# Optimization experiments

Measured on AMD Instinct MI355X. Metric: run time of the kernel, lower is better.

The kernel has to match this reference:

```python
import jax, jax.numpy as jnp
import numpy as np

WH, WW = 7, 7
SH, SW = 3, 3
NUM_HEADS = 8


def _rel_pos_index(wh, ww):
    coords = np.stack(np.meshgrid(np.arange(wh), np.arange(ww), indexing='ij')).reshape(2, -1)
    rel = (coords[:, :, None] - coords[:, None, :]).transpose(1, 2, 0)  # [N,N,2]
    rel[..., 0] += wh - 1
    rel[..., 1] += ww - 1
    rel[..., 0] *= 2 * ww - 1
    return rel.sum(-1)  # [N,N] int


def _attn_mask(Hp, Wp, wh, ww, sh, sw):
    img = np.zeros((Hp, Wp), dtype=np.float32)
    cnt = 0
    for hs in (slice(0, -wh), slice(-wh, -sh), slice(-sh, None)):
        for ws in (slice(0, -ww), slice(-ww, -sw), slice(-sw, None)):
            img[hs, ws] = cnt
            cnt += 1
    win = img.reshape(Hp // wh, wh, Wp // ww, ww).transpose(0, 2, 1, 3).reshape(-1, wh * ww)  # [nW,N]
    diff = win[:, None, :] - win[:, :, None]  # [nW,N,N]
    return np.where(diff != 0, -100.0, 0.0).astype(np.float32)


def _layernorm(x, g, b, eps=1e-5):
    mu = jnp.mean(x, -1, keepdims=True)
    var = jnp.mean(jnp.square(x - mu), -1, keepdims=True)
    return (x - mu) * jax.lax.rsqrt(var + eps) * g + b


def setup_inputs() -> dict:
    key = jax.random.key(0)
    ks = jax.random.split(key, 12)
    B, H, W, C = 32, 56, 56, 256
    hid = 4 * C
    s = lambda k, *shape: jax.random.normal(k, shape, jnp.float32) * 0.02
    return {
        'x': jax.random.normal(ks[0], (B, H * W, C), jnp.float32),
        'g1': jnp.ones((C,), jnp.float32), 'b1': jnp.zeros((C,), jnp.float32),
        'qkv_w': s(ks[1], 3 * C, C), 'qkv_b': jnp.zeros((3 * C,), jnp.float32),
        'bias_table': s(ks[2], (2 * WH - 1) * (2 * WW - 1), NUM_HEADS),
        'proj_w': s(ks[3], C, C), 'proj_b': jnp.zeros((C,), jnp.float32),
        'g2': jnp.ones((C,), jnp.float32), 'b2': jnp.zeros((C,), jnp.float32),
        'w1': s(ks[4], hid, C), 'bm1': jnp.zeros((hid,), jnp.float32),
        'w2': s(ks[5], C, hid), 'bm2': jnp.zeros((C,), jnp.float32),
        'H': H, 'W': W,
    }


def reference(x, g1, b1, qkv_w, qkv_b, bias_table, proj_w, proj_b, g2, b2, w1, bm1, w2, bm2, H, W):
    B, L, C = x.shape
    wh, ww = WH, WW
    nH = NUM_HEADS
    hd = C // nH
    scale = hd ** -0.5
    N = wh * ww

    shortcut = x
    h = _layernorm(x, g1, b1).reshape(B, H, W, C)
    pad_b = (wh - H % wh) % wh
    pad_r = (ww - W % ww) % ww
    if pad_b or pad_r:
        h = jnp.pad(h, ((0, 0), (0, pad_b), (0, pad_r), (0, 0)))
    Hp, Wp = h.shape[1], h.shape[2]

    h = jnp.roll(h, (-SH, -SW), axis=(1, 2))
    # window partition -> [B*nW, N, C]
    nWh, nWw = Hp // wh, Wp // ww
    xw = h.reshape(B, nWh, wh, nWw, ww, C).transpose(0, 1, 3, 2, 4, 5).reshape(-1, N, C)

    qkv = jnp.einsum('bnc,oc->bno', xw, qkv_w) + qkv_b  # [B*nW, N, 3C]
    qkv = qkv.reshape(-1, N, 3, nH, hd).transpose(2, 0, 3, 1, 4)
    q, k, v = qkv[0] * scale, qkv[1], qkv[2]  # [B*nW, nH, N, hd]
    attn = jnp.einsum('whnd,whmd->whnm', q, k)  # [B*nW, nH, N, N]

    rpi = jnp.asarray(_rel_pos_index(wh, ww))
    bias = bias_table[rpi.reshape(-1)].reshape(N, N, nH).transpose(2, 0, 1)  # [nH,N,N]
    attn = attn + bias[None]

    mask = jnp.asarray(_attn_mask(Hp, Wp, wh, ww, SH, SW))  # [nW,N,N]
    nW = mask.shape[0]
    attn = attn.reshape(B, nW, nH, N, N) + mask[None, :, None]
    attn = jax.nn.softmax(attn.reshape(-1, nH, N, N), axis=-1)

    out = jnp.einsum('whnm,whmd->whnd', attn, v).transpose(0, 2, 1, 3).reshape(-1, N, C)
    out = jnp.einsum('bnc,oc->bno', out, proj_w) + proj_b

    # window reverse
    out = out.reshape(B, nWh, nWw, wh, ww, C).transpose(0, 1, 3, 2, 4, 5).reshape(B, Hp, Wp, C)
    out = jnp.roll(out, (SH, SW), axis=(1, 2))
    if pad_b or pad_r:
        out = out[:, :H, :W, :]
    out = out.reshape(B, H * W, C)

    x = shortcut + out
    m = _layernorm(x, g2, b2)
    m = jax.nn.gelu(jnp.einsum('blc,oc->blo', m, w1) + bm1, approximate=False)
    m = jnp.einsum('blh,oh->blo', m, w2) + bm2
    return x + m
```

## Files before the change

kernel.cpp:

```cpp
#include <hip/hip_runtime.h>
#include <hip/hip_bf16.h>

#define DEVI __device__ __forceinline__
#define AS1 __attribute__((address_space(1)))
#define AS3 __attribute__((address_space(3)))

typedef short bf16x8 __attribute__((ext_vector_type(8)));
typedef float f32x4  __attribute__((ext_vector_type(4)));

constexpr int MROWS = 100352;

DEVI int win_row_to_token(int r) {
  int b   = r / 3136;
  int rem = r - b * 3136;
  int wi  = rem / 49;
  int t   = rem - wi * 49;
  int nwh = wi >> 3, nww = wi & 7;
  int th = t / 7, tw = t - th * 7;
  int h = nwh * 7 + th + 3; if (h >= 56) h -= 56;
  int w = nww * 7 + tw + 3; if (w >= 56) w -= 56;
  return b * 3136 + h * 56 + w;
}

DEVI unsigned short f2bf(float f) {
  __hip_bfloat16 h = __float2bfloat16(f);
  return __builtin_bit_cast(unsigned short, h);
}

__global__ void cvt_kernel(const float* __restrict__ in, __hip_bfloat16* __restrict__ out, int n) {
  int i = blockIdx.x * 256 + threadIdx.x;
  if (i < n) out[i] = __float2bfloat16(in[i]);
}

template<bool WIN>
__global__ __launch_bounds__(256) void ln_kernel(
    const float* __restrict__ xin, const float* __restrict__ g,
    const float* __restrict__ b, __hip_bfloat16* __restrict__ outb)
{
  int r = blockIdx.x * 4 + (threadIdx.x >> 6);
  int l = threadIdx.x & 63;
  int tok = WIN ? win_row_to_token(r) : r;
  float4 xv = *(const float4*)&xin[(size_t)tok * 256 + l * 4];
  float s = xv.x + xv.y + xv.z + xv.w;
  float q = xv.x * xv.x + xv.y * xv.y + xv.z * xv.z + xv.w * xv.w;
  #pragma unroll
  for (int off = 32; off; off >>= 1) { s += __shfl_xor(s, off); q += __shfl_xor(q, off); }
  float mu = s * (1.0f / 256.0f);
  float var = q * (1.0f / 256.0f) - mu * mu;
  float rs = rsqrtf(var + 1e-5f);
  float4 gv = *(const float4*)&g[l * 4];
  float4 bv = *(const float4*)&b[l * 4];
  ushort4 st;
  st.x = f2bf((xv.x - mu) * rs * gv.x + bv.x);
  st.y = f2bf((xv.y - mu) * rs * gv.y + bv.y);
  st.z = f2bf((xv.z - mu) * rs * gv.z + bv.z);
  st.w = f2bf((xv.w - mu) * rs * gv.w + bv.w);
  *(ushort4*)&outb[(size_t)r * 256 + l * 4] = st;
}

enum { EPI_QKV = 0, EPI_PROJ = 1, EPI_MLP1 = 2, EPI_MLP2 = 3 };

template<int EPI, int KTOT>
__global__ __launch_bounds__(512, 1) void strip3(
    const __hip_bfloat16* __restrict__ A,
    const __hip_bfloat16* __restrict__ Bw,
    int ntiles,
    const float* __restrict__ bias,
    const float* __restrict__ xres,
    float* __restrict__ outf,
    __hip_bfloat16* __restrict__ outb)
{
  constexpr int NKB = KTOT / 256;
  constexpr int NCH = NKB * 4;
  constexpr long TSTRIDE = 256L * KTOT * 2;
  __shared__ __align__(16) __hip_bfloat16 Bl[128 * 256];
  __shared__ __align__(16) __hip_bfloat16 Al[2][256 * 64];

  const int tid = threadIdx.x;
  const int w = tid >> 6, l = tid & 63;
  const int wr = w >> 1, wc = w & 1;
  const int g = l >> 4, lm = l & 15;

  const int xcd = blockIdx.x & 7;
  const int cu  = blockIdx.x >> 3;
  const int T   = 49 * ntiles;
  const int t0  = (cu * T) >> 5;
  const int t1  = ((cu + 1) * T) >> 5;

  char* AlB = (char*)&Al[0][0];
  char* BlB = (char*)&Bl[0];

  const int  dstW = w * 1024;
  const long aoff = (long)(w * 8 + (l >> 3)) * (KTOT * 2) + (((l & 7) ^ (l >> 3)) << 4);
  const int  bA   = wr * 8192  + lm * 128 + ((g ^ (lm & 7)) << 4);
  const int  bB   = wc * 32768 + lm * 512 + ((g ^ (lm & 7)) << 4);

  int nt = t0 / 49;
  int mtoff = t0 - nt * 49;
  const char* Ab = (const char*)A;
  const char* At = Ab + (long)(xcd * 49 + mtoff) * TSTRIDE;

  auto issueA = [&](const char* Atile, int coff, int buf) {
    #pragma unroll
    for (int j = 0; j < 4; ++j)
      __builtin_amdgcn_global_load_lds(
          (const AS1 void*)(Atile + aoff + j * (64L * KTOT * 2) + coff),
          (AS3 void*)(AlB + buf * 32768 + j * 8192 + dstW), 16, 0, 0);
  };
  auto stageB = [&](int nt_, int kb_) {
    const char* Bb = (const char*)(Bw + (size_t)nt_ * 128 * KTOT + kb_ * 256);
    #pragma unroll
    for (int j = 0; j < 8; ++j) {
      int U = j * 512 + w * 64 + l;
      int row = U >> 5;
      int su = (U & 31) ^ (row & 7);
      __builtin_amdgcn_global_load_lds(
          (const AS1 void*)(Bb + (long)row * (KTOT * 2) + su * 16),
          (AS3 void*)(BlB + j * 8192 + dstW), 16, 0, 0);
    }
  };

  stageB(nt, 0);
  int sBnt = nt, sBkb = 0;
  issueA(At, 0, 0);

  f32x4 acc[4][4];
  for (int t = t0; t < t1; ++t) {
    const bool wrap = (mtoff == 48);
    const char* Atn = wrap ? (Ab + (long)(xcd * 49) * TSTRIDE) : (At + TSTRIDE);
    #pragma unroll
    for (int mi = 0; mi < 4; ++mi)
      #pragma unroll
      for (int ni = 0; ni < 4; ++ni)
        acc[mi][ni] = f32x4{0.f, 0.f, 0.f, 0.f};

    #pragma unroll
    for (int kb = 0; kb < NKB; ++kb) {
      if (sBnt != nt || sBkb != kb) { stageB(nt, kb); sBnt = nt; sBkb = kb; }
      #pragma unroll
      for (int c = 0; c < 4; ++c) {
        const int chunk = kb * 4 + c;
        if (chunk == NCH - 1) {
          if (t == t1 - 1) {
            asm volatile("s_waitcnt vmcnt(0)" ::: "memory");
          } else {
            issueA(Atn, 0, 0);
            asm volatile("s_waitcnt vmcnt(4)" ::: "memory");
          }
        } else {
          issueA(At, (chunk + 1) * 128, (chunk + 1) & 1);
          asm volatile("s_waitcnt vmcnt(4)" ::: "memory");
        }
        __builtin_amdgcn_s_barrier();
        asm volatile("" ::: "memory");

        #pragma unroll
        for (int kk = 0; kk < 2; ++kk) {
          bf16x8 af[4], bf[4];
          const int ax = bA ^ (kk * 64);
          const int bx = bB ^ (kk * 64);
          #pragma unroll
          for (int mi = 0; mi < 4; ++mi)
            af[mi] = *(const bf16x8*)(AlB + (chunk & 1) * 32768 + ax + mi * 2048);
          #pragma unroll
          for (int ni = 0; ni < 4; ++ni)
            bf[ni] = *(const bf16x8*)(BlB + bx + c * 128 + ni * 8192);
          #pragma unroll
          for (int mi = 0; mi < 4; ++mi)
            #pragma unroll
            for (int ni = 0; ni < 4; ++ni)
              acc[mi][ni] = __builtin_amdgcn_mfma_f32_16x16x32_bf16(
                  af[mi], bf[ni], acc[mi][ni], 0, 0, 0);
        }
        asm volatile("" ::: "memory");
        __builtin_amdgcn_s_barrier();
      }
    }

    {
      const int mt = xcd * 49 + mtoff;
      #pragma unroll
      for (int mi = 0; mi < 4; ++mi)
        #pragma unroll
        for (int j = 0; j < 4; ++j) {
          int grow = mt * 256 + wr * 64 + mi * 16 + g * 4 + j;
          int orow = grow;
          if (EPI == EPI_PROJ) orow = win_row_to_token(grow);
          #pragma unroll
          for (int ni = 0; ni < 4; ++ni) {
            int gcol = nt * 128 + wc * 64 + ni * 16 + lm;
            float v = acc[mi][ni][j] + bias[gcol];
            if (EPI == EPI_QKV) {
              outb[(size_t)grow * 768 + gcol] = __float2bfloat16(v);
            } else if (EPI == EPI_PROJ) {
              size_t o = (size_t)orow * 256 + gcol;
              outf[o] = xres[o] + v;
            } else if (EPI == EPI_MLP1) {
              float u2 = v * (1.5957691216f + 0.1426930877f * v * v);
              float e  = __expf(u2);
              float ge = v * e / (e + 1.0f);
              outb[(size_t)grow * 1024 + gcol] = __float2bfloat16(ge);
            } else {
              size_t o = (size_t)grow * 256 + gcol;
              outf[o] += v;
            }
          }
        }
    }

    At = Atn;
    if (wrap) { mtoff = 0; ++nt; } else { ++mtoff; }
  }
}

__global__ __launch_bounds__(256) void bias_prep_kernel(
    const float* __restrict__ bt, float* __restrict__ Sadd)
{
  int blk = blockIdx.x;
  int cls = blk >> 3, h = blk & 7;
  int re = cls >> 1, ce = cls & 1;
  int lane = threadIdx.x & 63, fs = threadIdx.x >> 6;
  int g = lane >> 4, lm = lane & 15;
  #pragma unroll
  for (int i = 0; i < 4; ++i) {
    int f = fs * 4 + i;
    int mi = f >> 2, ni = f & 3;
    int key = ni * 16 + lm;
    f32x4 v;
    #pragma unroll
    for (int j = 0; j < 4; ++j) {
      int q = mi * 16 + g * 4 + j;
      float val;
      if (key >= 49) {
        val = -1e30f;
      } else {
        int qq = q > 48 ? 48 : q;
        int qh = qq / 7, qw = qq - qh * 7;
        int kh = key / 7, kw = key - kh * 7;
        int rpi = (qh - kh + 6) * 13 + (qw - kw + 6);
        val = bt[rpi * 8 + h];
        int rq = (re ? (qh < 4 ? 1 : 2) : 0) * 3 + (ce ? (qw < 4 ? 1 : 2) : 0);
        int rk = (re ? (kh < 4 ? 1 : 2) : 0) * 3 + (ce ? (kw < 4 ? 1 : 2) : 0);
        if (rq != rk) val -= 100.0f;
      }
      v[j] = val;
    }
    ((f32x4*)Sadd)[(blk * 16 + f) * 64 + lane] = v;
  }
}

__global__ __launch_bounds__(256) void attn_mfma_kernel(
    const __hip_bfloat16* __restrict__ qkv,
    const float* __restrict__ Sadd,
    __hip_bfloat16* __restrict__ attn_out)
{
  __shared__ __align__(16) __hip_bfloat16 Pl[4][64 * 72];
  int blk = blockIdx.x;
  int win = blk >> 1, half = blk & 1;
  int w = threadIdx.x >> 6, l = threadIdx.x & 63;
  int head = half * 4 + w;
  int g = l >> 4, lm = l & 15;
  int wi = win & 63;
  int cls = (((wi >> 3) == 7) ? 2 : 0) | (((wi & 7) == 7) ? 1 : 0);
  const __hip_bfloat16* base = qkv + (size_t)win * 49 * 768 + head * 32;

  bf16x8 aQ[4], bK[4];
  #pragma unroll
  for (int mi = 0; mi < 4; ++mi) {
    int q = mi * 16 + lm; if (q > 48) q = 48;
    aQ[mi] = *(const bf16x8*)(base + q * 768 + g * 8);
  }
  #pragma unroll
  for (int ni = 0; ni < 4; ++ni) {
    int k = ni * 16 + lm; if (k > 48) k = 48;
    bK[ni] = *(const bf16x8*)(base + 256 + k * 768 + g * 8);
  }
  f32x4 acc[4][4] = {};
  #pragma unroll
  for (int mi = 0; mi < 4; ++mi)
    #pragma unroll
    for (int ni = 0; ni < 4; ++ni)
      acc[mi][ni] = __builtin_amdgcn_mfma_f32_16x16x32_bf16(aQ[mi], bK[ni], acc[mi][ni], 0, 0, 0);

  const float scale = 0.17677669529663687f;
  const f32x4* Sb = (const f32x4*)Sadd + (size_t)(cls * 8 + head) * 16 * 64 + l;

  f32x4 rsum[4];
  __hip_bfloat16* P = Pl[w];
  #pragma unroll
  for (int mi = 0; mi < 4; ++mi) {
    #pragma unroll
    for (int ni = 0; ni < 4; ++ni) {
      f32x4 sv = Sb[(mi * 4 + ni) * 64];
      #pragma unroll
      for (int j = 0; j < 4; ++j) acc[mi][ni][j] = acc[mi][ni][j] * scale + sv[j];
    }
    f32x4 mx = acc[mi][0];
    #pragma unroll
    for (int ni = 1; ni < 4; ++ni)
      #pragma unroll
      for (int j = 0; j < 4; ++j) mx[j] = fmaxf(mx[j], acc[mi][ni][j]);
    #pragma unroll
    for (int msk = 1; msk < 16; msk <<= 1)
      #pragma unroll
      for (int j = 0; j < 4; ++j) mx[j] = fmaxf(mx[j], __shfl_xor(mx[j], msk));
    f32x4 sm = {};
    #pragma unroll
    for (int ni = 0; ni < 4; ++ni)
      #pragma unroll
      for (int j = 0; j < 4; ++j) {
        float e = __expf(acc[mi][ni][j] - mx[j]);
        acc[mi][ni][j] = e;
        sm[j] += e;
      }
    #pragma unroll
    for (int msk = 1; msk < 16; msk <<= 1)
      #pragma unroll
      for (int j = 0; j < 4; ++j) sm[j] += __shfl_xor(sm[j], msk);
    rsum[mi] = sm;
    #pragma unroll
    for (int ni = 0; ni < 4; ++ni)
      #pragma unroll
      for (int j = 0; j < 4; ++j) {
        int q = mi * 16 + g * 4 + j;
        int key = ni * 16 + lm;
        P[q * 72 + key] = __float2bfloat16(acc[mi][ni][j]);
      }
  }

  bf16x8 bV[2][2];
  #pragma unroll
  for (int s = 0; s < 2; ++s)
    #pragma unroll
    for (int n2 = 0; n2 < 2; ++n2) {
      bf16x8 vv;
      #pragma unroll
      for (int e = 0; e < 8; ++e) {
        int key = s * 32 + g * 8 + e; if (key > 48) key = 48;
        vv[e] = __builtin_bit_cast(short, base[512 + key * 768 + n2 * 16 + lm]);
      }
      bV[s][n2] = vv;
    }

  f32x4 o[4][2] = {};
  #pragma unroll
  for (int s = 0; s < 2; ++s)
    #pragma unroll
    for (int mi2 = 0; mi2 < 4; ++mi2) {
      bf16x8 aP = *(const bf16x8*)&P[(mi2 * 16 + lm) * 72 + s * 32 + g * 8];
      #pragma unroll
      for (int n2 = 0; n2 < 2; ++n2)
        o[mi2][n2] = __builtin_amdgcn_mfma_f32_16x16x32_bf16(aP, bV[s][n2], o[mi2][n2], 0, 0, 0);
    }

  #pragma unroll
  for (int mi2 = 0; mi2 < 4; ++mi2) {
    f32x4 li;
    #pragma unroll
    for (int j = 0; j < 4; ++j) li[j] = 1.0f / rsum[mi2][j];
    #pragma unroll
    for (int n2 = 0; n2 < 2; ++n2)
      #pragma unroll
      for (int j = 0; j < 4; ++j) {
        int q = mi2 * 16 + g * 4 + j;
        if (q < 49)
          attn_out[((size_t)win * 49 + q) * 256 + head * 32 + n2 * 16 + lm] =
              __float2bfloat16(o[mi2][n2][j] * li[j]);
      }
  }
}

extern "C" void kernel_launch(void* const* d_in, const int* in_sizes, int n_in,
                              void* d_out, int out_size, void* d_ws, size_t ws_size,
                              hipStream_t stream) {
  const float* x          = (const float*)d_in[0];
  const float* g1         = (const float*)d_in[1];
  const float* b1         = (const float*)d_in[2];
  const float* qkv_w      = (const float*)d_in[3];
  const float* qkv_b      = (const float*)d_in[4];
  const float* bias_table = (const float*)d_in[5];
  const float* proj_w     = (const float*)d_in[6];
  const float* proj_b     = (const float*)d_in[7];
  const float* g2         = (const float*)d_in[8];
  const float* b2         = (const float*)d_in[9];
  const float* w1         = (const float*)d_in[10];
  const float* bm1        = (const float*)d_in[11];
  const float* w2         = (const float*)d_in[12];
  const float* bm2        = (const float*)d_in[13];
  float* out = (float*)d_out;

  char* ws = (char*)d_ws;
  __hip_bfloat16* A_ln   = (__hip_bfloat16*)(ws);
  __hip_bfloat16* qkvb   = (__hip_bfloat16*)(ws + 51380224);
  __hip_bfloat16* attn_o = (__hip_bfloat16*)(ws + 205520896);
  __hip_bfloat16* hidden = qkvb;
  __hip_bfloat16* qkv_wb  = (__hip_bfloat16*)(ws + 256901120);
  __hip_bfloat16* proj_wb = qkv_wb + 196608;
  __hip_bfloat16* w1b     = proj_wb + 65536;
  __hip_bfloat16* w2b     = w1b + 262144;
  float* Sadd = (float*)(ws + 258473984);

  cvt_kernel<<<(196608 + 255) / 256, 256, 0, stream>>>(qkv_w, qkv_wb, 196608);
  cvt_kernel<<<(65536  + 255) / 256, 256, 0, stream>>>(proj_w, proj_wb, 65536);
  cvt_kernel<<<(262144 + 255) / 256, 256, 0, stream>>>(w1, w1b, 262144);
  cvt_kernel<<<(262144 + 255) / 256, 256, 0, stream>>>(w2, w2b, 262144);
  bias_prep_kernel<<<32, 256, 0, stream>>>(bias_table, Sadd);

  ln_kernel<true><<<MROWS / 4, 256, 0, stream>>>(x, g1, b1, A_ln);

  strip3<EPI_QKV, 256><<<256, 512, 0, stream>>>(
      A_ln, qkv_wb, 6, qkv_b, nullptr, nullptr, qkvb);

  attn_mfma_kernel<<<4096, 256, 0, stream>>>(qkvb, Sadd, attn_o);

  strip3<EPI_PROJ, 256><<<256, 512, 0, stream>>>(
      attn_o, proj_wb, 2, proj_b, x, out, nullptr);

  ln_kernel<false><<<MROWS / 4, 256, 0, stream>>>(out, g2, b2, A_ln);

  strip3<EPI_MLP1, 256><<<256, 512, 0, stream>>>(
      A_ln, w1b, 8, bm1, nullptr, nullptr, hidden);

  strip3<EPI_MLP2, 1024><<<256, 512, 0, stream>>>(
      hidden, w2b, 2, bm2, nullptr, out, nullptr);
}
```

Measured before the change: 498.7 us.

## Shrink GEMM strip tiles to 128 rows with 256-thread blocks, single-buffered A

The persistent strip GEMM goes from 512-thread blocks with 256-row M tiles to 256-thread blocks with 128-row tiles, launched as 512 blocks so two can share a CU. The A tile is now single-buffered. The wait is a full vmcnt(0) plus barrier before each chunk, and the next chunk's loads (and the next B strip) are issued only after compute finishes. The aim is overlap across co-resident blocks rather than within one block, with smaller LDS per block. The cost is that latency is no longer hidden inside a block, and B is re-staged more often relative to the work done.

```diff
diff --git a/kernel.cpp b/kernel.cpp
--- a/kernel.cpp
+++ b/kernel.cpp
@@ -61,7 +61,7 @@
 enum { EPI_QKV = 0, EPI_PROJ = 1, EPI_MLP1 = 2, EPI_MLP2 = 3 };
 
 template<int EPI, int KTOT>
-__global__ __launch_bounds__(512, 1) void strip3(
+__global__ __launch_bounds__(256) void strip4(
     const __hip_bfloat16* __restrict__ A,
     const __hip_bfloat16* __restrict__ Bw,
     int ntiles,
@@ -72,9 +72,10 @@
 {
   constexpr int NKB = KTOT / 256;
   constexpr int NCH = NKB * 4;
-  constexpr long TSTRIDE = 256L * KTOT * 2;
+  constexpr int K2  = KTOT * 2;
+  constexpr long TSTRIDE = 128L * K2;
   __shared__ __align__(16) __hip_bfloat16 Bl[128 * 256];
-  __shared__ __align__(16) __hip_bfloat16 Al[2][256 * 64];
+  __shared__ __align__(16) __hip_bfloat16 Al[128 * 64];
 
   const int tid = threadIdx.x;
   const int w = tid >> 6, l = tid & 63;
@@ -82,52 +83,49 @@
   const int g = l >> 4, lm = l & 15;
 
   const int xcd = blockIdx.x & 7;
-  const int cu  = blockIdx.x >> 3;
-  const int T   = 49 * ntiles;
-  const int t0  = (cu * T) >> 5;
-  const int t1  = ((cu + 1) * T) >> 5;
-
-  char* AlB = (char*)&Al[0][0];
-  char* BlB = (char*)&Bl[0];
+  const int cu2 = blockIdx.x >> 3;
+  const int T   = 98 * ntiles;
+  const int t0  = (cu2 * T) >> 6;
+  const int t1  = ((cu2 + 1) * T) >> 6;
+
+  char* AlB = (char*)Al;
+  char* BlB = (char*)Bl;
 
   const int  dstW = w * 1024;
-  const long aoff = (long)(w * 8 + (l >> 3)) * (KTOT * 2) + (((l & 7) ^ (l >> 3)) << 4);
-  const int  bA   = wr * 8192  + lm * 128 + ((g ^ (lm & 7)) << 4);
-  const int  bB   = wc * 32768 + lm * 512 + ((g ^ (lm & 7)) << 4);
-
-  int nt = t0 / 49;
-  int mtoff = t0 - nt * 49;
-  const char* Ab = (const char*)A;
-  const char* At = Ab + (long)(xcd * 49 + mtoff) * TSTRIDE;
-
-  auto issueA = [&](const char* Atile, int coff, int buf) {
+  const long aoff = (long)(tid >> 3) * K2 + (((tid & 7) ^ ((tid >> 3) & 7)) << 4);
+  const long boff = (long)(tid >> 5) * K2 + (((tid & 31) ^ ((tid >> 5) & 7)) << 4);
+  const int  bA = (wr * 64 + lm) * 128 + ((g ^ (lm & 7)) << 4);
+  const int  bB = (wc * 64 + lm) * 512 + ((g ^ (lm & 7)) << 4);
+
+  int nt = t0 / 98;
+  int mtoff = t0 - nt * 98;
+  const char* Ab = (const char*)A + (long)xcd * 98 * TSTRIDE;
+  const char* At = Ab + (long)mtoff * TSTRIDE;
+
+  auto issueA = [&](const char* Atile, int ch) {
     #pragma unroll
     for (int j = 0; j < 4; ++j)
       __builtin_amdgcn_global_load_lds(
-          (const AS1 void*)(Atile + aoff + j * (64L * KTOT * 2) + coff),
-          (AS3 void*)(AlB + buf * 32768 + j * 8192 + dstW), 16, 0, 0);
+          (const AS1 void*)(Atile + aoff + j * (32L * K2) + ch * 128),
+          (AS3 void*)(AlB + j * 4096 + dstW), 16, 0, 0);
   };
   auto stageB = [&](int nt_, int kb_) {
-    const char* Bb = (const char*)(Bw + (size_t)nt_ * 128 * KTOT + kb_ * 256);
-    #pragma unroll
-    for (int j = 0; j < 8; ++j) {
-      int U = j * 512 + w * 64 + l;
-      int row = U >> 5;
-      int su = (U & 31) ^ (row & 7);
+    const char* Bb = (const char*)Bw + (long)nt_ * 128 * K2 + kb_ * 512;
+    #pragma unroll
+    for (int j = 0; j < 16; ++j)
       __builtin_amdgcn_global_load_lds(
-          (const AS1 void*)(Bb + (long)row * (KTOT * 2) + su * 16),
-          (AS3 void*)(BlB + j * 8192 + dstW), 16, 0, 0);
-    }
+          (const AS1 void*)(Bb + boff + j * (8L * K2)),
+          (AS3 void*)(BlB + j * 4096 + dstW), 16, 0, 0);
   };
 
   stageB(nt, 0);
-  int sBnt = nt, sBkb = 0;
-  issueA(At, 0, 0);
+  issueA(At, 0);
 
   f32x4 acc[4][4];
   for (int t = t0; t < t1; ++t) {
-    const bool wrap = (mtoff == 48);
-    const char* Atn = wrap ? (Ab + (long)(xcd * 49) * TSTRIDE) : (At + TSTRIDE);
+    const bool wrap = (mtoff == 97);
+    const char* Atn = wrap ? Ab : (At + TSTRIDE);
+    const int ntn = wrap ? nt + 1 : nt;
     #pragma unroll
     for (int mi = 0; mi < 4; ++mi)
       #pragma unroll
@@ -136,35 +134,24 @@
 
     #pragma unroll
     for (int kb = 0; kb < NKB; ++kb) {
-      if (sBnt != nt || sBkb != kb) { stageB(nt, kb); sBnt = nt; sBkb = kb; }
-      #pragma unroll
-      for (int c = 0; c < 4; ++c) {
-        const int chunk = kb * 4 + c;
-        if (chunk == NCH - 1) {
-          if (t == t1 - 1) {
-            asm volatile("s_waitcnt vmcnt(0)" ::: "memory");
-          } else {
-            issueA(Atn, 0, 0);
-            asm volatile("s_waitcnt vmcnt(4)" ::: "memory");
-          }
-        } else {
-          issueA(At, (chunk + 1) * 128, (chunk + 1) & 1);
-          asm volatile("s_waitcnt vmcnt(4)" ::: "memory");
-        }
+      #pragma unroll
+      for (int c4 = 0; c4 < 4; ++c4) {
+        const int ch = kb * 4 + c4;
+        asm volatile("s_waitcnt vmcnt(0)" ::: "memory");
         __builtin_amdgcn_s_barrier();
         asm volatile("" ::: "memory");
 
         #pragma unroll
         for (int kk = 0; kk < 2; ++kk) {
           bf16x8 af[4], bf[4];
-          const int ax = bA ^ (kk * 64);
-          const int bx = bB ^ (kk * 64);
+          const int ax = bA ^ (kk << 6);
+          const int bx = bB ^ (kk << 6);
           #pragma unroll
           for (int mi = 0; mi < 4; ++mi)
-            af[mi] = *(const bf16x8*)(AlB + (chunk & 1) * 32768 + ax + mi * 2048);
+            af[mi] = *(const bf16x8*)(AlB + ax + mi * 2048);
           #pragma unroll
           for (int ni = 0; ni < 4; ++ni)
-            bf[ni] = *(const bf16x8*)(BlB + bx + c * 128 + ni * 8192);
+            bf[ni] = *(const bf16x8*)(BlB + bx + c4 * 128 + ni * 8192);
           #pragma unroll
           for (int mi = 0; mi < 4; ++mi)
             #pragma unroll
@@ -172,18 +159,27 @@
               acc[mi][ni] = __builtin_amdgcn_mfma_f32_16x16x32_bf16(
                   af[mi], bf[ni], acc[mi][ni], 0, 0, 0);
         }
+
         asm volatile("" ::: "memory");
         __builtin_amdgcn_s_barrier();
+        if (ch < NCH - 1) {
+          if (NKB > 1 && c4 == 3) stageB(nt, kb + 1);
+          issueA(At, ch + 1);
+        } else if (t < t1 - 1) {
+          if (NKB > 1) stageB(ntn, 0);
+          else if (ntn != nt) stageB(ntn, 0);
+          issueA(Atn, 0);
+        }
       }
     }
 
     {
-      const int mt = xcd * 49 + mtoff;
+      const int mt = xcd * 98 + mtoff;
       #pragma unroll
       for (int mi = 0; mi < 4; ++mi)
         #pragma unroll
         for (int j = 0; j < 4; ++j) {
-          int grow = mt * 256 + wr * 64 + mi * 16 + g * 4 + j;
+          int grow = mt * 128 + wr * 64 + mi * 16 + g * 4 + j;
           int orow = grow;
           if (EPI == EPI_PROJ) orow = win_row_to_token(grow);
           #pragma unroll
@@ -209,7 +205,7 @@
     }
 
     At = Atn;
-    if (wrap) { mtoff = 0; ++nt; } else { ++mtoff; }
+    if (wrap) { mtoff = 0; nt = ntn; } else { ++mtoff; }
   }
 }
 
@@ -408,19 +404,19 @@
 
   ln_kernel<true><<<MROWS / 4, 256, 0, stream>>>(x, g1, b1, A_ln);
 
-  strip3<EPI_QKV, 256><<<256, 512, 0, stream>>>(
+  strip4<EPI_QKV, 256><<<512, 256, 0, stream>>>(
       A_ln, qkv_wb, 6, qkv_b, nullptr, nullptr, qkvb);
 
   attn_mfma_kernel<<<4096, 256, 0, stream>>>(qkvb, Sadd, attn_o);
 
-  strip3<EPI_PROJ, 256><<<256, 512, 0, stream>>>(
+  strip4<EPI_PROJ, 256><<<512, 256, 0, stream>>>(
       attn_o, proj_wb, 2, proj_b, x, out, nullptr);
 
   ln_kernel<false><<<MROWS / 4, 256, 0, stream>>>(out, g2, b2, A_ln);
 
-  strip3<EPI_MLP1, 256><<<256, 512, 0, stream>>>(
+  strip4<EPI_MLP1, 256><<<512, 256, 0, stream>>>(
       A_ln, w1b, 8, bm1, nullptr, nullptr, hidden);
 
-  strip3<EPI_MLP2, 1024><<<256, 512, 0, stream>>>(
+  strip4<EPI_MLP2, 1024><<<512, 256, 0, stream>>>(
       hidden, w2b, 2, bm2, nullptr, out, nullptr);
 }
```

After: 499.7 us. No clear change (+0.2%).
